# Kernel tuning notes

Measured on AMD Instinct MI355X. Metric: run time of the kernel, lower is better.

Reference implementation:

```python
import jax, jax.numpy as jnp
from jax import lax
import numpy as np

B, T, C = 8, 16384, 64
NUM_FILTERS, FILTER_SIZE = 64, 5
LEAKY_SLOPE = 0.3  # keras activation 'leaky_relu' default negative_slope


def setup_inputs() -> dict:
    key = jax.random.key(0)
    k1, k2, k3 = jax.random.split(key, 3)
    x = jax.random.normal(k1, (B, T, C), dtype=jnp.float32)
    interp_weights = jax.random.normal(k2, (C,), dtype=jnp.float32)
    # Conv1D kernel layout: [filter_size, in_channels, out_channels]
    conv_kernel = jax.random.normal(k3, (FILTER_SIZE, C, NUM_FILTERS), dtype=jnp.float32) * 0.05
    conv_bias = jnp.zeros((NUM_FILTERS,), dtype=jnp.float32)
    return {"x": x, "interp_weights": interp_weights,
            "conv_kernel": conv_kernel, "conv_bias": conv_bias}


def reference(x, interp_weights, conv_kernel, conv_bias):
    # Sigmoid gate per channel
    w = jax.nn.sigmoid(interp_weights)  # [C]
    # The diag conv2d (filter [1,2,C,C], SAME) is: blend[t] = w*x[t] + (1-w)*x[t+1]
    # (TF SAME for even width pads one zero frame on the right)
    x_next = jnp.concatenate([x[:, 1:, :], jnp.zeros_like(x[:, :1, :])], axis=1)
    blend = w * x + (1.0 - w) * x_next  # [B, T, C]
    # Interleave: even positions original, odd positions blended -> [B, 2T, C]
    up = jnp.stack([x, blend], axis=2).reshape(B, 2 * T, C)
    # Conv1D(num_filters, filter_size, padding='same', stride 1) + leaky_relu
    y = lax.conv_general_dilated(
        up, conv_kernel,
        window_strides=(1,), padding='SAME',
        dimension_numbers=('NWC', 'WIO', 'NWC'))
    y = y + conv_bias
    return jnp.where(y >= 0, y, LEAKY_SLOPE * y)
```

## Files before the change

kernel.cpp:

```cpp
#include <hip/hip_runtime.h>
#include <hip/hip_bf16.h>
#include <cstdint>


#define T_ 16384
#define TWO_T 32768
#define NFR 68

typedef __bf16 bf16x8 __attribute__((ext_vector_type(8)));
typedef float  f32x4  __attribute__((ext_vector_type(4)));
typedef unsigned short u16x8 __attribute__((ext_vector_type(8)));

__device__ __forceinline__ float sigmoidf_(float z) {
    return 1.0f / (1.0f + expf(-z));
}

__device__ __forceinline__ unsigned short f2bf(float f) {
    union { float f; uint32_t u; } v; v.f = f;
    uint32_t u = v.u;
    return (unsigned short)((u + 0x7FFFu + ((u >> 16) & 1u)) >> 16);
}

__global__ void lu_prep_kernel(const float* __restrict__ iw,
                               const float* __restrict__ ck,
                               const float* __restrict__ x,
                               unsigned short* __restrict__ bp,
                               float* __restrict__ corrf,
                               float* __restrict__ zp) {
    int fi = blockIdx.x;
    int l  = threadIdx.x;
    if (fi < 56) {
        int phase, ks, nt;
        if (fi < 24) { phase = 0; ks = fi >> 2; nt = fi & 3; }
        else         { phase = 1; ks = (fi - 24) >> 2; nt = (fi - 24) & 3; }
        int tap = ks >> 1;
        int n   = nt * 16 + (l & 15);
        int c0  = ((ks & 1) << 5) + ((l >> 4) << 3);
        u16x8 pk;
#pragma unroll
        for (int i = 0; i < 8; ++i) {
            int c = c0 + i;
            float w = sigmoidf_(iw[c]);
            float v;
            #define CK(k) ck[((k) * 64 + c) * 64 + n]
            if (phase == 0) {
                if (tap == 0)      v = CK(0) + w * CK(1);
                else if (tap == 1) v = (1.f - w) * CK(1) + CK(2) + w * CK(3);
                else               v = (1.f - w) * CK(3) + CK(4);
            } else {
                if (tap == 0)      v = w * CK(0);
                else if (tap == 1) v = (1.f - w) * CK(0) + CK(1) + w * CK(2);
                else if (tap == 2) v = (1.f - w) * CK(2) + CK(3) + w * CK(4);
                else               v = (1.f - w) * CK(4);
            }
            #undef CK
            pk[i] = f2bf(v);
        }
        *(u16x8*)(bp + (((size_t)fi * 64) + l) * 8) = pk;
    } else {
        int b = fi - 56;
        int f = l;
        float cE = 0.f, cO = 0.f;
#pragma unroll
        for (int c = 0; c < 64; ++c) {
            float w = sigmoidf_(iw[c]);
            float g = (1.f - w) * x[(size_t)b * T_ * 64 + c];
            cE += ck[(64 + c) * 64 + f] * g;
            cO += ck[c * 64 + f] * g;
        }
        corrf[b * 128 + f]      = cE;
        corrf[b * 128 + 64 + f] = cO;
        if (fi == 63) zp[l] = 0.f;
    }
}

__device__ __forceinline__ void gload16(const float* g, float* l) {
    __builtin_amdgcn_global_load_lds(
        (const __attribute__((address_space(1))) uint32_t*)g,
        (__attribute__((address_space(3))) uint32_t*)l, 16, 0, 0);
}

__device__ __forceinline__ bf16x8 pack8(f32x4 a, f32x4 b) {
    bf16x8 r;
    r[0] = (__bf16)a[0]; r[1] = (__bf16)a[1];
    r[2] = (__bf16)a[2]; r[3] = (__bf16)a[3];
    r[4] = (__bf16)b[0]; r[5] = (__bf16)b[1];
    r[6] = (__bf16)b[2]; r[7] = (__bf16)b[3];
    return r;
}

__global__ __launch_bounds__(256, 4) void lu_main_kernel(
        const float* __restrict__ x,
        const unsigned short* __restrict__ bp,
        const float* __restrict__ corrf,
        const float* __restrict__ bias,
        const float* __restrict__ zp,
        float* __restrict__ out) {
    __shared__ __align__(16) float xl[NFR * 64];

    const int bid  = blockIdx.x;
    const int b    = bid >> 8;
    const int q    = bid & 255;
    const int p0   = q << 6;
    const int lane = threadIdx.x & 63;
    const int wv   = threadIdx.x >> 6;

    const float* xb = x + (size_t)b * T_ * 64;

    bf16x8 We[6], Wo[8];
#pragma unroll
    for (int ks = 0; ks < 6; ++ks)
        We[ks] = __builtin_bit_cast(bf16x8,
            *(const u16x8*)(bp + (((size_t)(ks * 4 + wv)) * 64 + lane) * 8));
#pragma unroll
    for (int ks = 0; ks < 8; ++ks)
        Wo[ks] = __builtin_bit_cast(bf16x8,
            *(const u16x8*)(bp + (((size_t)(24 + ks * 4 + wv)) * 64 + lane) * 8));

    const int hi   = lane >> 4;
    const int hi2  = hi << 1;
    const int col  = lane & 15;
    const float4 bias4 = *(const float4*)(bias + (wv << 4) + (hi << 2));

#pragma unroll
    for (int g = 0; g < 5; ++g) {
        int j0 = g * 16 + (wv << 2);
        if (j0 < NFR) {
            int j  = j0 + (lane >> 4);
            int gf = p0 - 1 + j;
            int ch = (lane & 15) ^ (j & 7);
            const float* gp = ((unsigned)gf < (unsigned)T_)
                            ? xb + ((size_t)gf << 6) + (ch << 2)
                            : zp + (ch << 2);
            gload16(gp, xl + j0 * 64);
        }
    }

    __syncthreads();

    const char* xwb = (const char*)xl;

#pragma unroll
    for (int w = 0; w < 4; ++w) {
        f32x4 accE = {0.f, 0.f, 0.f, 0.f};
        f32x4 accO = {0.f, 0.f, 0.f, 0.f};
#pragma unroll
        for (int tap = 0; tap < 4; ++tap) {
            int j    = (w << 4) + col + tap;
            int key  = j & 7;
            int off0 = (j << 8) + ((hi2 ^ key) << 4);
            f32x4 qa = *(const f32x4*)(xwb + off0);
            f32x4 qb = *(const f32x4*)(xwb + (off0 ^ 16));
            f32x4 qc = *(const f32x4*)(xwb + off0 + 128);
            f32x4 qd = *(const f32x4*)(xwb + ((off0 + 128) ^ 16));
            bf16x8 x0 = pack8(qa, qb);
            bf16x8 x1 = pack8(qc, qd);
            if (tap < 3) {
                accE = __builtin_amdgcn_mfma_f32_16x16x32_bf16(We[tap * 2],     x0, accE, 0, 0, 0);
                accE = __builtin_amdgcn_mfma_f32_16x16x32_bf16(We[tap * 2 + 1], x1, accE, 0, 0, 0);
            }
            accO = __builtin_amdgcn_mfma_f32_16x16x32_bf16(Wo[tap * 2],     x0, accO, 0, 0, 0);
            accO = __builtin_amdgcn_mfma_f32_16x16x32_bf16(Wo[tap * 2 + 1], x1, accO, 0, 0, 0);
        }

        if (((q | w) == 0) && col == 0) {
            const float4 cE4 = *(const float4*)(corrf + b * 128 + (wv << 4) + (hi << 2));
            const float4 cO4 = *(const float4*)(corrf + b * 128 + 64 + (wv << 4) + (hi << 2));
            accE[0] -= cE4.x; accE[1] -= cE4.y; accE[2] -= cE4.z; accE[3] -= cE4.w;
            accO[0] -= cO4.x; accO[1] -= cO4.y; accO[2] -= cO4.z; accO[3] -= cO4.w;
        }

        const int tl = p0 + (w << 4) + col;
        const size_t fbase = ((size_t)b * TWO_T + ((size_t)tl << 1)) * 64
                           + (wv << 4) + (hi << 2);
        float4 vE, vO;
        {
            float e0 = accE[0] + bias4.x, e1 = accE[1] + bias4.y,
                  e2 = accE[2] + bias4.z, e3 = accE[3] + bias4.w;
            vE.x = e0 >= 0.f ? e0 : 0.3f * e0;
            vE.y = e1 >= 0.f ? e1 : 0.3f * e1;
            vE.z = e2 >= 0.f ? e2 : 0.3f * e2;
            vE.w = e3 >= 0.f ? e3 : 0.3f * e3;
            float o0 = accO[0] + bias4.x, o1 = accO[1] + bias4.y,
                  o2 = accO[2] + bias4.z, o3 = accO[3] + bias4.w;
            vO.x = o0 >= 0.f ? o0 : 0.3f * o0;
            vO.y = o1 >= 0.f ? o1 : 0.3f * o1;
            vO.z = o2 >= 0.f ? o2 : 0.3f * o2;
            vO.w = o3 >= 0.f ? o3 : 0.3f * o3;
        }
        *(float4*)(out + fbase)      = vE;
        *(float4*)(out + fbase + 64) = vO;
    }
}

extern "C" void kernel_launch(void* const* d_in, const int* in_sizes, int n_in,
                              void* d_out, int out_size, void* d_ws, size_t ws_size,
                              hipStream_t stream) {
    (void)in_sizes; (void)n_in; (void)out_size; (void)ws_size;
    const float* x    = (const float*)d_in[0];
    const float* iw   = (const float*)d_in[1];
    const float* ck   = (const float*)d_in[2];
    const float* bias = (const float*)d_in[3];
    float* out = (float*)d_out;
    unsigned short* bp = (unsigned short*)d_ws;
    float* corrf = (float*)((char*)d_ws + 57344);
    float* zp    = (float*)((char*)d_ws + 61440);

    lu_prep_kernel<<<64, 64, 0, stream>>>(iw, ck, x, bp, corrf, zp);
    lu_main_kernel<<<2048, 256, 0, stream>>>(x, bp, corrf, bias, zp, out);
}
```

Baseline: 32.02 us.

## Double-buffer two 64-step tiles per block and overlap second load with compute

Each block now handles 128 time steps instead of 64, split into two stages with separate LDS buffers. The second stage's global-to-LDS load is issued before the first stage's compute and waited on through vmcnt counters, so memory latency overlaps with MFMA work and the per-block weight register load is amortised over twice the work. In exchange the grid is halved, LDS per block grows, and there are extra padding rows, so occupancy and parallelism drop.

```diff
diff --git a/kernel.cpp b/kernel.cpp
--- a/kernel.cpp
+++ b/kernel.cpp
@@ -5,7 +5,7 @@
 
 #define T_ 16384
 #define TWO_T 32768
-#define NFR 68
+#define BROWS 80
 
 typedef __bf16 bf16x8 __attribute__((ext_vector_type(8)));
 typedef float  f32x4  __attribute__((ext_vector_type(4)));
@@ -96,12 +96,12 @@
         const float* __restrict__ bias,
         const float* __restrict__ zp,
         float* __restrict__ out) {
-    __shared__ __align__(16) float xl[NFR * 64];
+    __shared__ __align__(16) float xl[2 * BROWS * 64];
 
     const int bid  = blockIdx.x;
-    const int b    = bid >> 8;
-    const int q    = bid & 255;
-    const int p0   = q << 6;
+    const int b    = bid >> 7;
+    const int q    = bid & 127;
+    const int p0   = q << 7;
     const int lane = threadIdx.x & 63;
     const int wv   = threadIdx.x >> 6;
 
@@ -122,75 +122,91 @@
     const int col  = lane & 15;
     const float4 bias4 = *(const float4*)(bias + (wv << 4) + (hi << 2));
 
-#pragma unroll
-    for (int g = 0; g < 5; ++g) {
-        int j0 = g * 16 + (wv << 2);
-        if (j0 < NFR) {
-            int j  = j0 + (lane >> 4);
-            int gf = p0 - 1 + j;
-            int ch = (lane & 15) ^ (j & 7);
-            const float* gp = ((unsigned)gf < (unsigned)T_)
-                            ? xb + ((size_t)gf << 6) + (ch << 2)
-                            : zp + (ch << 2);
-            gload16(gp, xl + j0 * 64);
-        }
+    #define STAGE(buf, ps)                                                  \
+    {                                                                       \
+        _Pragma("unroll")                                                   \
+        for (int k = 0; k < 5; ++k) {                                       \
+            int j0 = (wv << 2) + (k << 4);                                  \
+            int j  = j0 + (lane >> 4);                                      \
+            int t  = (ps) - 8 + j;                                          \
+            int ch = (lane & 15) ^ (j & 7);                                 \
+            const float* gp = ((unsigned)t < (unsigned)T_)                  \
+                            ? xb + ((size_t)t << 6) + (ch << 2)             \
+                            : zp + (ch << 2);                               \
+            gload16(gp, xl + (((buf) * BROWS) + j0) * 64);                  \
+        }                                                                   \
     }
 
-    __syncthreads();
-
-    const char* xwb = (const char*)xl;
-
-#pragma unroll
-    for (int w = 0; w < 4; ++w) {
-        f32x4 accE = {0.f, 0.f, 0.f, 0.f};
-        f32x4 accO = {0.f, 0.f, 0.f, 0.f};
-#pragma unroll
-        for (int tap = 0; tap < 4; ++tap) {
-            int j    = (w << 4) + col + tap;
-            int key  = j & 7;
-            int off0 = (j << 8) + ((hi2 ^ key) << 4);
-            f32x4 qa = *(const f32x4*)(xwb + off0);
-            f32x4 qb = *(const f32x4*)(xwb + (off0 ^ 16));
-            f32x4 qc = *(const f32x4*)(xwb + off0 + 128);
-            f32x4 qd = *(const f32x4*)(xwb + ((off0 + 128) ^ 16));
-            bf16x8 x0 = pack8(qa, qb);
-            bf16x8 x1 = pack8(qc, qd);
-            if (tap < 3) {
-                accE = __builtin_amdgcn_mfma_f32_16x16x32_bf16(We[tap * 2],     x0, accE, 0, 0, 0);
-                accE = __builtin_amdgcn_mfma_f32_16x16x32_bf16(We[tap * 2 + 1], x1, accE, 0, 0, 0);
-            }
-            accO = __builtin_amdgcn_mfma_f32_16x16x32_bf16(Wo[tap * 2],     x0, accO, 0, 0, 0);
-            accO = __builtin_amdgcn_mfma_f32_16x16x32_bf16(Wo[tap * 2 + 1], x1, accO, 0, 0, 0);
-        }
-
-        if (((q | w) == 0) && col == 0) {
-            const float4 cE4 = *(const float4*)(corrf + b * 128 + (wv << 4) + (hi << 2));
-            const float4 cO4 = *(const float4*)(corrf + b * 128 + 64 + (wv << 4) + (hi << 2));
-            accE[0] -= cE4.x; accE[1] -= cE4.y; accE[2] -= cE4.z; accE[3] -= cE4.w;
-            accO[0] -= cO4.x; accO[1] -= cO4.y; accO[2] -= cO4.z; accO[3] -= cO4.w;
-        }
-
-        const int tl = p0 + (w << 4) + col;
-        const size_t fbase = ((size_t)b * TWO_T + ((size_t)tl << 1)) * 64
-                           + (wv << 4) + (hi << 2);
-        float4 vE, vO;
-        {
-            float e0 = accE[0] + bias4.x, e1 = accE[1] + bias4.y,
-                  e2 = accE[2] + bias4.z, e3 = accE[3] + bias4.w;
-            vE.x = e0 >= 0.f ? e0 : 0.3f * e0;
-            vE.y = e1 >= 0.f ? e1 : 0.3f * e1;
-            vE.z = e2 >= 0.f ? e2 : 0.3f * e2;
-            vE.w = e3 >= 0.f ? e3 : 0.3f * e3;
-            float o0 = accO[0] + bias4.x, o1 = accO[1] + bias4.y,
-                  o2 = accO[2] + bias4.z, o3 = accO[3] + bias4.w;
-            vO.x = o0 >= 0.f ? o0 : 0.3f * o0;
-            vO.y = o1 >= 0.f ? o1 : 0.3f * o1;
-            vO.z = o2 >= 0.f ? o2 : 0.3f * o2;
-            vO.w = o3 >= 0.f ? o3 : 0.3f * o3;
-        }
-        *(float4*)(out + fbase)      = vE;
-        *(float4*)(out + fbase + 64) = vO;
+    STAGE(0, p0)
+
+#pragma unroll
+    for (int s = 0; s < 2; ++s) {
+        const int ps = p0 + (s << 6);
+
+        if (s == 0) {
+            STAGE(1, p0 + 64)
+            asm volatile("s_waitcnt vmcnt(5)" ::: "memory");
+        } else {
+            asm volatile("s_waitcnt vmcnt(0)" ::: "memory");
+        }
+        __builtin_amdgcn_s_barrier();
+        __builtin_amdgcn_sched_barrier(0);
+
+        const char* xwb = (const char*)(xl + s * (BROWS * 64));
+
+#pragma unroll
+        for (int w = 0; w < 4; ++w) {
+            f32x4 accE = {0.f, 0.f, 0.f, 0.f};
+            f32x4 accO = {0.f, 0.f, 0.f, 0.f};
+#pragma unroll
+            for (int tap = 0; tap < 4; ++tap) {
+                int j    = (w << 4) + col + tap + 7;
+                int key  = j & 7;
+                int off0 = (j << 8) + ((hi2 ^ key) << 4);
+                f32x4 qa = *(const f32x4*)(xwb + off0);
+                f32x4 qb = *(const f32x4*)(xwb + (off0 ^ 16));
+                f32x4 qc = *(const f32x4*)(xwb + off0 + 128);
+                f32x4 qd = *(const f32x4*)(xwb + ((off0 + 128) ^ 16));
+                bf16x8 x0 = pack8(qa, qb);
+                bf16x8 x1 = pack8(qc, qd);
+                if (tap < 3) {
+                    accE = __builtin_amdgcn_mfma_f32_16x16x32_bf16(We[tap * 2],     x0, accE, 0, 0, 0);
+                    accE = __builtin_amdgcn_mfma_f32_16x16x32_bf16(We[tap * 2 + 1], x1, accE, 0, 0, 0);
+                }
+                accO = __builtin_amdgcn_mfma_f32_16x16x32_bf16(Wo[tap * 2],     x0, accO, 0, 0, 0);
+                accO = __builtin_amdgcn_mfma_f32_16x16x32_bf16(Wo[tap * 2 + 1], x1, accO, 0, 0, 0);
+            }
+
+            if (((q | s | w) == 0) && col == 0) {
+                const float4 cE4 = *(const float4*)(corrf + b * 128 + (wv << 4) + (hi << 2));
+                const float4 cO4 = *(const float4*)(corrf + b * 128 + 64 + (wv << 4) + (hi << 2));
+                accE[0] -= cE4.x; accE[1] -= cE4.y; accE[2] -= cE4.z; accE[3] -= cE4.w;
+                accO[0] -= cO4.x; accO[1] -= cO4.y; accO[2] -= cO4.z; accO[3] -= cO4.w;
+            }
+
+            const int tl = ps + (w << 4) + col;
+            const size_t fbase = ((size_t)b * TWO_T + ((size_t)tl << 1)) * 64
+                               + (wv << 4) + (hi << 2);
+            float4 vE, vO;
+            {
+                float e0 = accE[0] + bias4.x, e1 = accE[1] + bias4.y,
+                      e2 = accE[2] + bias4.z, e3 = accE[3] + bias4.w;
+                vE.x = e0 >= 0.f ? e0 : 0.3f * e0;
+                vE.y = e1 >= 0.f ? e1 : 0.3f * e1;
+                vE.z = e2 >= 0.f ? e2 : 0.3f * e2;
+                vE.w = e3 >= 0.f ? e3 : 0.3f * e3;
+                float o0 = accO[0] + bias4.x, o1 = accO[1] + bias4.y,
+                      o2 = accO[2] + bias4.z, o3 = accO[3] + bias4.w;
+                vO.x = o0 >= 0.f ? o0 : 0.3f * o0;
+                vO.y = o1 >= 0.f ? o1 : 0.3f * o1;
+                vO.z = o2 >= 0.f ? o2 : 0.3f * o2;
+                vO.w = o3 >= 0.f ? o3 : 0.3f * o3;
+            }
+            *(float4*)(out + fbase)      = vE;
+            *(float4*)(out + fbase + 64) = vO;
+        }
     }
+    #undef STAGE
 }
 
 extern "C" void kernel_launch(void* const* d_in, const int* in_sizes, int n_in,
@@ -207,5 +223,5 @@
     float* zp    = (float*)((char*)d_ws + 61440);
 
     lu_prep_kernel<<<64, 64, 0, stream>>>(iw, ck, x, bp, corrf, zp);
-    lu_main_kernel<<<2048, 256, 0, stream>>>(x, bp, corrf, bias, zp, out);
-}
+    lu_main_kernel<<<1024, 256, 0, stream>>>(x, bp, corrf, bias, zp, out);
+}
```

After: 32.58 us. Within noise of the previous version (+1.7%).

## Split even and odd output phases across separate waves with 512-thread blocks

Applied to the files above, without the earlier changes.

Each block now runs 8 waves: four handle the even-phase outputs and four handle the odd-phase outputs, where previously each wave computed both. This halves the per-wave weight registers and accumulators and doubles the waves available to hide latency. The cost is that each LDS frame is read and packed to bf16 twice, once per phase, and the even waves do less work than the odd ones, so the load is unbalanced.

```diff
diff --git a/kernel.cpp b/kernel.cpp
--- a/kernel.cpp
+++ b/kernel.cpp
@@ -89,7 +89,7 @@
     return r;
 }
 
-__global__ __launch_bounds__(256, 4) void lu_main_kernel(
+__global__ __launch_bounds__(512, 8) void lu_main_kernel(
         const float* __restrict__ x,
         const unsigned short* __restrict__ bp,
         const float* __restrict__ corrf,
@@ -102,30 +102,32 @@
     const int b    = bid >> 8;
     const int q    = bid & 255;
     const int p0   = q << 6;
-    const int lane = threadIdx.x & 63;
-    const int wv   = threadIdx.x >> 6;
+    const int tid  = threadIdx.x;
+    const int lane = tid & 63;
+    const int wv   = tid >> 6;
+    const int ph   = wv >> 2;
+    const int ft   = wv & 3;
 
     const float* xb = x + (size_t)b * T_ * 64;
 
-    bf16x8 We[6], Wo[8];
-#pragma unroll
-    for (int ks = 0; ks < 6; ++ks)
-        We[ks] = __builtin_bit_cast(bf16x8,
-            *(const u16x8*)(bp + (((size_t)(ks * 4 + wv)) * 64 + lane) * 8));
+    bf16x8 W[8];
+    const int fb0 = ph ? 24 : 0;
 #pragma unroll
     for (int ks = 0; ks < 8; ++ks)
-        Wo[ks] = __builtin_bit_cast(bf16x8,
-            *(const u16x8*)(bp + (((size_t)(24 + ks * 4 + wv)) * 64 + lane) * 8));
+        if (ph || ks < 6)
+            W[ks] = __builtin_bit_cast(bf16x8,
+                *(const u16x8*)(bp + (((size_t)(fb0 + ks * 4 + ft)) * 64 + lane) * 8));
 
     const int hi   = lane >> 4;
     const int hi2  = hi << 1;
     const int col  = lane & 15;
-    const float4 bias4 = *(const float4*)(bias + (wv << 4) + (hi << 2));
-
-#pragma unroll
-    for (int g = 0; g < 5; ++g) {
-        int j0 = g * 16 + (wv << 2);
-        if (j0 < NFR) {
+    const float4 bias4 = *(const float4*)(bias + (ft << 4) + (hi << 2));
+
+#pragma unroll
+    for (int g = 0; g < 3; ++g) {
+        int G = wv + (g << 3);
+        if (G < 17) {
+            int j0 = G << 2;
             int j  = j0 + (lane >> 4);
             int gf = p0 - 1 + j;
             int ch = (lane & 15) ^ (j & 7);
@@ -142,54 +144,43 @@
 
 #pragma unroll
     for (int w = 0; w < 4; ++w) {
-        f32x4 accE = {0.f, 0.f, 0.f, 0.f};
-        f32x4 accO = {0.f, 0.f, 0.f, 0.f};
+        f32x4 acc = {0.f, 0.f, 0.f, 0.f};
 #pragma unroll
         for (int tap = 0; tap < 4; ++tap) {
-            int j    = (w << 4) + col + tap;
-            int key  = j & 7;
-            int off0 = (j << 8) + ((hi2 ^ key) << 4);
-            f32x4 qa = *(const f32x4*)(xwb + off0);
-            f32x4 qb = *(const f32x4*)(xwb + (off0 ^ 16));
-            f32x4 qc = *(const f32x4*)(xwb + off0 + 128);
-            f32x4 qd = *(const f32x4*)(xwb + ((off0 + 128) ^ 16));
-            bf16x8 x0 = pack8(qa, qb);
-            bf16x8 x1 = pack8(qc, qd);
-            if (tap < 3) {
-                accE = __builtin_amdgcn_mfma_f32_16x16x32_bf16(We[tap * 2],     x0, accE, 0, 0, 0);
-                accE = __builtin_amdgcn_mfma_f32_16x16x32_bf16(We[tap * 2 + 1], x1, accE, 0, 0, 0);
+            if (ph || tap < 3) {
+                int j    = (w << 4) + col + tap;
+                int key  = j & 7;
+                int off0 = (j << 8) + ((hi2 ^ key) << 4);
+                f32x4 qa = *(const f32x4*)(xwb + off0);
+                f32x4 qb = *(const f32x4*)(xwb + (off0 ^ 16));
+                bf16x8 x0 = pack8(qa, qb);
+                acc = __builtin_amdgcn_mfma_f32_16x16x32_bf16(W[tap * 2], x0, acc, 0, 0, 0);
+                f32x4 qc = *(const f32x4*)(xwb + off0 + 128);
+                f32x4 qd = *(const f32x4*)(xwb + ((off0 + 128) ^ 16));
+                bf16x8 x1 = pack8(qc, qd);
+                acc = __builtin_amdgcn_mfma_f32_16x16x32_bf16(W[tap * 2 + 1], x1, acc, 0, 0, 0);
             }
-            accO = __builtin_amdgcn_mfma_f32_16x16x32_bf16(Wo[tap * 2],     x0, accO, 0, 0, 0);
-            accO = __builtin_amdgcn_mfma_f32_16x16x32_bf16(Wo[tap * 2 + 1], x1, accO, 0, 0, 0);
         }
 
         if (((q | w) == 0) && col == 0) {
-            const float4 cE4 = *(const float4*)(corrf + b * 128 + (wv << 4) + (hi << 2));
-            const float4 cO4 = *(const float4*)(corrf + b * 128 + 64 + (wv << 4) + (hi << 2));
-            accE[0] -= cE4.x; accE[1] -= cE4.y; accE[2] -= cE4.z; accE[3] -= cE4.w;
-            accO[0] -= cO4.x; accO[1] -= cO4.y; accO[2] -= cO4.z; accO[3] -= cO4.w;
+            const float4 c4 = *(const float4*)(corrf + b * 128 + (ph << 6)
+                                               + (ft << 4) + (hi << 2));
+            acc[0] -= c4.x; acc[1] -= c4.y; acc[2] -= c4.z; acc[3] -= c4.w;
         }
 
         const int tl = p0 + (w << 4) + col;
-        const size_t fbase = ((size_t)b * TWO_T + ((size_t)tl << 1)) * 64
-                           + (wv << 4) + (hi << 2);
-        float4 vE, vO;
+        const size_t fbase = ((size_t)b * TWO_T + (size_t)((tl << 1) + ph)) * 64
+                           + (ft << 4) + (hi << 2);
+        float4 v;
         {
-            float e0 = accE[0] + bias4.x, e1 = accE[1] + bias4.y,
-                  e2 = accE[2] + bias4.z, e3 = accE[3] + bias4.w;
-            vE.x = e0 >= 0.f ? e0 : 0.3f * e0;
-            vE.y = e1 >= 0.f ? e1 : 0.3f * e1;
-            vE.z = e2 >= 0.f ? e2 : 0.3f * e2;
-            vE.w = e3 >= 0.f ? e3 : 0.3f * e3;
-            float o0 = accO[0] + bias4.x, o1 = accO[1] + bias4.y,
-                  o2 = accO[2] + bias4.z, o3 = accO[3] + bias4.w;
-            vO.x = o0 >= 0.f ? o0 : 0.3f * o0;
-            vO.y = o1 >= 0.f ? o1 : 0.3f * o1;
-            vO.z = o2 >= 0.f ? o2 : 0.3f * o2;
-            vO.w = o3 >= 0.f ? o3 : 0.3f * o3;
-        }
-        *(float4*)(out + fbase)      = vE;
-        *(float4*)(out + fbase + 64) = vO;
+            float e0 = acc[0] + bias4.x, e1 = acc[1] + bias4.y,
+                  e2 = acc[2] + bias4.z, e3 = acc[3] + bias4.w;
+            v.x = e0 >= 0.f ? e0 : 0.3f * e0;
+            v.y = e1 >= 0.f ? e1 : 0.3f * e1;
+            v.z = e2 >= 0.f ? e2 : 0.3f * e2;
+            v.w = e3 >= 0.f ? e3 : 0.3f * e3;
+        }
+        *(float4*)(out + fbase) = v;
     }
 }
 
@@ -207,5 +198,5 @@
     float* zp    = (float*)((char*)d_ws + 61440);
 
     lu_prep_kernel<<<64, 64, 0, stream>>>(iw, ck, x, bp, corrf, zp);
-    lu_main_kernel<<<2048, 256, 0, stream>>>(x, bp, corrf, bias, zp, out);
-}
+    lu_main_kernel<<<2048, 512, 0, stream>>>(x, bp, corrf, bias, zp, out);
+}
```

Measured after the change: 39.98 us. 24.9% more time.
